# Kernel tuning notes

Hardware: AMD Instinct MI355X
Metric: run time of the kernel (lower is better)

Reference implementation:

```python
import jax, jax.numpy as jnp
import numpy as np

N_ENT = 50000
N_EDGE = 500000
H_DIM = 128
N_REL_TAB = 475  # 2*n_rel + 1


def setup_inputs() -> dict:
    key = jax.random.key(0)
    ks = jax.random.split(key, 8)
    scale = 1.0 / np.sqrt(H_DIM)
    return {
        "ent_emb": jax.random.normal(ks[0], (N_ENT, H_DIM), jnp.float32) * scale,
        "rel_emb": jax.random.normal(ks[1], (N_REL_TAB, H_DIM), jnp.float32) * scale,
        "w_edge": jax.random.normal(ks[2], (H_DIM, H_DIM), jnp.float32) * scale,
        "w_node": jax.random.normal(ks[3], (H_DIM, H_DIM), jnp.float32) * scale,
        "w_comp": jax.random.normal(ks[4], (H_DIM, H_DIM), jnp.float32) * scale,
        "src": jax.random.randint(ks[5], (N_EDGE,), 0, N_ENT, jnp.int32),
        "dst": jax.random.randint(ks[6], (N_EDGE,), 0, N_ENT, jnp.int32),
        "rel_id": jax.random.randint(ks[7], (N_EDGE,), 0, N_REL_TAB - 1, jnp.int32),
    }


def _edge_softmax(logits, dst, n_nodes):
    # dgl.ops.edge_softmax: softmax over incoming edges of each destination node
    m = jax.ops.segment_max(logits, dst, num_segments=n_nodes)  # (N,)
    ex = jnp.exp(logits - m[dst])                               # (E,)
    s = jax.ops.segment_sum(ex, dst, num_segments=n_nodes)     # (N,)
    return ex / s[dst]


def _attn_aggregate(msg, key_emb_dst, dst, n_nodes, w):
    # norm = e_dot_v, edge_softmax, weighted scatter-sum, GEMM, Tanh
    logits = jnp.sum(msg * key_emb_dst, axis=-1)                # (E,)
    a = _edge_softmax(logits, dst, n_nodes)                     # (E,)
    neigh = jax.ops.segment_sum(msg * a[:, None], dst, num_segments=n_nodes)  # (N,H)
    return jnp.tanh(neigh @ w)


def reference(ent_emb, rel_emb, w_edge, w_node, w_comp, src, dst, rel_id):
    n = ent_emb.shape[0]
    v = ent_emb[dst]            # (E,H) destination node emb (shared key for all layers)
    u = ent_emb[src]            # (E,H)
    r = rel_emb[rel_id]         # (E,H)

    # EdgeLayer: message = rel emb
    edge_out = _attn_aggregate(r, v, dst, n, w_edge)
    # NodeLayer: message = src node emb (u_dot_v logits, u_mul_e aggregation)
    node_out = _attn_aggregate(u, v, dst, n, w_node)
    # CompLayer (comp_op='add'): message = u + rel emb
    comp_out = _attn_aggregate(u + r, v, dst, n, w_comp)

    return ent_emb + edge_out + node_out + comp_out
```

## Files before the change

kernel.cpp:

```cpp
#include <hip/hip_runtime.h>
#include <math.h>

#define N_ENT   50000
#define N_REL   475
#define N_EDGE  500000
#define HD      128
#define CAP     64

typedef unsigned int u32;
typedef __attribute__((ext_vector_type(8))) short short8;
typedef __attribute__((ext_vector_type(4))) float f32x4;
typedef __attribute__((ext_vector_type(2))) float f32x2;
typedef __attribute__((ext_vector_type(4))) u32 u32x4;

__device__ __forceinline__ u32 bf16_1(float f) {
  u32 u = __float_as_uint(f);
  return (u + 0x7fffu + ((u >> 16) & 1u)) >> 16;
}
__device__ __forceinline__ u32 bf16_pack(float lo, float hi) {
  return bf16_1(lo) | (bf16_1(hi) << 16);
}
__device__ __forceinline__ float bf_lo(u32 w) { return __uint_as_float(w << 16); }
__device__ __forceinline__ float bf_hi(u32 w) { return __uint_as_float(w & 0xffff0000u); }
__device__ __forceinline__ f32x2 bf2(u32 w) { return (f32x2){bf_lo(w), bf_hi(w)}; }
__device__ __forceinline__ float fast_tanh(float x) {
  float e = __expf(2.f * x);
  return 1.f - 2.f * __builtin_amdgcn_rcpf(e + 1.f);
}

#define DEG_BLKS ((N_EDGE + 255) / 256)
#define CVT_ITEMS ((N_ENT + N_REL) * 16 + 3 * 8 * 4 * 64)
#define CVT_BLKS ((CVT_ITEMS + 255) / 256)

__global__ void k_degree_cvt(const int* __restrict__ dst, const int* __restrict__ src,
                             const int* __restrict__ rel, int* __restrict__ counts,
                             u32* __restrict__ psru,
                             const float* __restrict__ ent, const float* __restrict__ relw,
                             const float* __restrict__ we, const float* __restrict__ wn,
                             const float* __restrict__ wc, u32* __restrict__ ent16,
                             u32* __restrict__ rel16, u32* __restrict__ wpack) {
  int b = blockIdx.x;
  if (b < DEG_BLKS) {
    int e = b * 256 + threadIdx.x;
    if (e < N_EDGE) {
      int d = dst[e];
      int slot = atomicAdd(&counts[d], 1);
      if (slot > CAP - 1) slot = CAP - 1;
      psru[(size_t)d * CAP + slot] = (u32)src[e] | ((u32)rel[e] << 16);
    }
    return;
  }
  int t = (b - DEG_BLKS) * 256 + threadIdx.x;
  const int CVT = (N_ENT + N_REL) * 16;
  if (t < CVT) {
    int row = t >> 4, seg = t & 15;
    const float* s;
    u32* d;
    if (row < N_ENT) {
      s = ent + (size_t)row * HD + seg * 8;
      d = ent16 + (size_t)row * 64 + seg * 4;
    } else {
      int rr = row - N_ENT;
      s = relw + (size_t)rr * HD + seg * 8;
      d = rel16 + (size_t)rr * 64 + seg * 4;
    }
    float4 A = *(const float4*)s, B = *(const float4*)(s + 4);
    u32x4 o = {bf16_pack(A.x, A.y), bf16_pack(A.z, A.w),
               bf16_pack(B.x, B.y), bf16_pack(B.z, B.w)};
    *(u32x4*)d = o;
  } else if (t < CVT_ITEMS) {
    int idx = t - CVT;
    int lane = idx & 63, ks = (idx >> 6) & 3, ct = (idx >> 8) & 7, l = idx >> 11;
    const float* W = (l == 0) ? we : (l == 1) ? wn : wc;
    int c = ct * 16 + (lane & 15);
    int kb = ks * 32 + (lane >> 4) * 8;
    u32x4 o;
#pragma unroll
    for (int jp = 0; jp < 4; ++jp) {
      int k0 = kb + 2 * jp;
      o[jp] = bf16_pack(W[k0 * HD + c], W[(k0 + 1) * HD + c]);
    }
    *(u32x4*)(wpack + idx * 4) = o;
  }
}

__global__ __launch_bounds__(256) void k_aggregate(
    const u32* __restrict__ ent16, const u32* __restrict__ rel16,
    const int* __restrict__ counts, const u32* __restrict__ psru,
    u32* __restrict__ neighb) {
  int lane = threadIdx.x & 63;
  int node = blockIdx.x * 4 + (threadIdx.x >> 6);
  int grp = lane >> 4, gl = lane & 15;

  u32x4 V = *(const u32x4*)(ent16 + (size_t)node * 64 + gl * 4);
  f32x2 vv2[4];
#pragma unroll
  for (int k = 0; k < 4; ++k) vv2[k] = bf2(V[k]);

  f32x2 Su = {0.f, 0.f};
  float S2 = 0.f;
  f32x2 a0[4], a1[4], a2[4];
#pragma unroll
  for (int k = 0; k < 4; ++k) a0[k] = a1[k] = a2[k] = (f32x2){0.f, 0.f};

  int cnt = counts[node];
  if (cnt > CAP) cnt = CAP;
  int e0 = node * CAP, e1 = e0 + cnt;
  if (e0 < e1) {
    int elast = e1 - 1;
    auto fetch = [&](int eb, u32x4& U, u32x4& R) {
      int e = eb + grp;
      u32 p = psru[(e < e1) ? e : elast];
      U = *(const u32x4*)(ent16 + (size_t)(p & 0xFFFFu) * 64 + gl * 4);
      R = *(const u32x4*)(rel16 + (size_t)(p >> 16) * 64 + gl * 4);
    };
    auto process = [&](u32x4& U, u32x4& R, int eb) {
      f32x2 cu2[4], cr2[4];
#pragma unroll
      for (int k = 0; k < 4; ++k) { cu2[k] = bf2(U[k]); cr2[k] = bf2(R[k]); }
      fetch(eb + 12, U, R);
      bool valid = (eb + grp < e1);
      f32x2 du2 = {0.f, 0.f}, dq2 = {0.f, 0.f};
#pragma unroll
      for (int k = 0; k < 4; ++k) {
        du2 += cu2[k] * vv2[k];
        dq2 += cr2[k] * vv2[k];
      }
      f32x2 p = {du2.x + du2.y, dq2.x + dq2.y};
#pragma unroll
      for (int off = 1; off < 16; off <<= 1) {
        f32x2 t;
        t.x = __shfl_xor(p.x, off, 64);
        t.y = __shfl_xor(p.y, off, 64);
        p += t;
      }
      float e_u = valid ? __expf(p.x) : 0.f;
      float e_r = valid ? __expf(p.y) : 0.f;
      float e_c = e_u * e_r;
      Su += (f32x2){e_r, e_u};
      S2 += e_c;
      f32x2 er2 = {e_r, e_r}, eu2 = {e_u, e_u}, ec2 = {e_c, e_c};
#pragma unroll
      for (int k = 0; k < 4; ++k) {
        a0[k] += er2 * cr2[k];
        a1[k] += eu2 * cu2[k];
        a2[k] += ec2 * (cu2[k] + cr2[k]);
      }
    };
    u32x4 uA, rA, uB, rB, uC, rC;
    fetch(e0, uA, rA);
    fetch(e0 + 4, uB, rB);
    fetch(e0 + 8, uC, rC);
    int eb = e0;
    for (; eb + 8 < e1; eb += 12) {
      process(uA, rA, eb);
      process(uB, rB, eb + 4);
      process(uC, rC, eb + 8);
    }
    if (eb < e1) process(uA, rA, eb);
    if (eb + 4 < e1) process(uB, rB, eb + 4);
  }

  {
    f32x2 t;
    t.x = __shfl_xor(Su.x, 16, 64); t.y = __shfl_xor(Su.y, 16, 64); Su += t;
    t.x = __shfl_xor(Su.x, 32, 64); t.y = __shfl_xor(Su.y, 32, 64); Su += t;
    S2 += __shfl_xor(S2, 16, 64); S2 += __shfl_xor(S2, 32, 64);
  }
  float w0 = (Su.x > 0.f) ? __builtin_amdgcn_rcpf(Su.x) : 0.f;
  float w1 = (Su.y > 0.f) ? __builtin_amdgcn_rcpf(Su.y) : 0.f;
  float w2 = (S2 > 0.f) ? __builtin_amdgcn_rcpf(S2) : 0.f;
#pragma unroll
  for (int k = 0; k < 4; ++k) {
    f32x2 t;
    t.x = __shfl_xor(a0[k].x, 16, 64); t.y = __shfl_xor(a0[k].y, 16, 64); a0[k] += t;
    t.x = __shfl_xor(a0[k].x, 32, 64); t.y = __shfl_xor(a0[k].y, 32, 64); a0[k] += t;
    t.x = __shfl_xor(a1[k].x, 16, 64); t.y = __shfl_xor(a1[k].y, 16, 64); a1[k] += t;
    t.x = __shfl_xor(a1[k].x, 32, 64); t.y = __shfl_xor(a1[k].y, 32, 64); a1[k] += t;
    t.x = __shfl_xor(a2[k].x, 16, 64); t.y = __shfl_xor(a2[k].y, 16, 64); a2[k] += t;
    t.x = __shfl_xor(a2[k].x, 32, 64); t.y = __shfl_xor(a2[k].y, 32, 64); a2[k] += t;
  }

  int base = node * 64 + gl * 4;
  if (grp == 0) {
    u32x4 o = {bf16_pack(a0[0].x * w0, a0[0].y * w0), bf16_pack(a0[1].x * w0, a0[1].y * w0),
               bf16_pack(a0[2].x * w0, a0[2].y * w0), bf16_pack(a0[3].x * w0, a0[3].y * w0)};
    *(u32x4*)(neighb + base) = o;
  } else if (grp == 1) {
    u32x4 o = {bf16_pack(a1[0].x * w1, a1[0].y * w1), bf16_pack(a1[1].x * w1, a1[1].y * w1),
               bf16_pack(a1[2].x * w1, a1[2].y * w1), bf16_pack(a1[3].x * w1, a1[3].y * w1)};
    *(u32x4*)(neighb + N_ENT * 64 + base) = o;
  } else if (grp == 2) {
    u32x4 o = {bf16_pack(a2[0].x * w2, a2[0].y * w2), bf16_pack(a2[1].x * w2, a2[1].y * w2),
               bf16_pack(a2[2].x * w2, a2[2].y * w2), bf16_pack(a2[3].x * w2, a2[3].y * w2)};
    *(u32x4*)(neighb + 2 * N_ENT * 64 + base) = o;
  }
}

__global__ __launch_bounds__(256) void k_out(
    const float* __restrict__ ent, const u32* __restrict__ neighb,
    const u32* __restrict__ wpack, float* __restrict__ out) {
  int lane = threadIdx.x & 63, wv = threadIdx.x >> 6;
  int n0 = blockIdx.x * 64 + wv * 16;

  int arow = n0 + (lane & 15);
  int arow_c = (arow < N_ENT) ? arow : 0;
  int ko2 = (lane >> 4) * 4;

  f32x4 res[8];
#pragma unroll
  for (int t = 0; t < 8; ++t) res[t] = (f32x4){0.f, 0.f, 0.f, 0.f};

#pragma unroll
  for (int l = 0; l < 3; ++l) {
    const u32* nb = neighb + (size_t)l * (N_ENT * 64);
    short8 a[4];
#pragma unroll
    for (int ks = 0; ks < 4; ++ks)
      a[ks] = *(const short8*)(nb + (size_t)arow_c * 64 + ks * 16 + ko2);
    const u32* wp = wpack + l * 8192;
#pragma unroll
    for (int ct = 0; ct < 8; ++ct) {
      f32x4 acc = (f32x4){0.f, 0.f, 0.f, 0.f};
#pragma unroll
      for (int ks = 0; ks < 4; ++ks) {
        short8 b = *(const short8*)(wp + ((ct * 4 + ks) * 64 + lane) * 4);
        acc = __builtin_amdgcn_mfma_f32_16x16x32_bf16(a[ks], b, acc, 0, 0, 0);
      }
#pragma unroll
      for (int r = 0; r < 4; ++r) res[ct][r] += fast_tanh(acc[r]);
    }
  }
  int rbase = n0 + (lane >> 4) * 4;
  int cbase = lane & 15;
#pragma unroll
  for (int ct = 0; ct < 8; ++ct) {
    int col = ct * 16 + cbase;
#pragma unroll
    for (int r = 0; r < 4; ++r) {
      int row = rbase + r;
      if (row < N_ENT)
        out[(size_t)row * HD + col] = ent[(size_t)row * HD + col] + res[ct][r];
    }
  }
}

extern "C" void kernel_launch(void* const* d_in, const int* in_sizes, int n_in,
                              void* d_out, int out_size, void* d_ws, size_t ws_size,
                              hipStream_t stream) {
  const float* ent = (const float*)d_in[0];
  const float* rel = (const float*)d_in[1];
  const float* w_e = (const float*)d_in[2];
  const float* w_n = (const float*)d_in[3];
  const float* w_c = (const float*)d_in[4];
  const int* src = (const int*)d_in[5];
  const int* dst = (const int*)d_in[6];
  const int* relid = (const int*)d_in[7];
  float* out = (float*)d_out;

  char* ws = (char*)d_ws;
  size_t off = 0;
  auto alloc = [&](size_t bytes) {
    void* p = ws + off;
    off = (off + bytes + 255) & ~(size_t)255;
    return p;
  };
  int* counts = (int*)alloc((size_t)N_ENT * 4);
  u32* psru = (u32*)alloc((size_t)N_ENT * CAP * 4);
  u32* ent16 = (u32*)alloc((size_t)N_ENT * 64 * 4);
  u32* rel16 = (u32*)alloc((size_t)N_REL * 64 * 4);
  u32* neighb = (u32*)alloc(3ull * N_ENT * 64 * 4);
  u32* wpack = (u32*)alloc((size_t)3 * 8 * 4 * 64 * 4 * 4);
  (void)ws_size; (void)in_sizes; (void)n_in; (void)out_size;

  hipMemsetAsync(counts, 0, (size_t)N_ENT * 4, stream);

  k_degree_cvt<<<DEG_BLKS + CVT_BLKS, 256, 0, stream>>>(dst, src, relid, counts, psru,
                                                        ent, rel, w_e, w_n, w_c, ent16,
                                                        rel16, wpack);
  k_aggregate<<<N_ENT / 4, 256, 0, stream>>>(ent16, rel16, counts, psru, neighb);
  k_out<<<(N_ENT + 63) / 64, 256, 0, stream>>>(ent, neighb, wpack, out);
}
```

Measured before the change: 215.4 us.

## Fuse neighbor aggregation and output GEMM into one kernel via LDS slab

Merges the aggregation kernel and the MFMA output kernel into a single kernel. Each wave now aggregates 16 nodes one after another and stages their bf16 neighbor sums in a padded LDS slab, then runs the three GEMMs with tanh straight from LDS. This removes the global write and re-read of the intermediate neighbor buffer and one kernel launch. In exchange, far fewer waves are in flight to hide gather latency, and the odd LDS stride breaks 16-byte alignment of the vector LDS accesses.

```diff
diff --git a/kernel.cpp b/kernel.cpp
--- a/kernel.cpp
+++ b/kernel.cpp
@@ -31,6 +31,7 @@
 #define DEG_BLKS ((N_EDGE + 255) / 256)
 #define CVT_ITEMS ((N_ENT + N_REL) * 16 + 3 * 8 * 4 * 64)
 #define CVT_BLKS ((CVT_ITEMS + 255) / 256)
+#define NSTRIDE 193
 
 __global__ void k_degree_cvt(const int* __restrict__ dst, const int* __restrict__ src,
                              const int* __restrict__ rel, int* __restrict__ counts,
@@ -84,128 +85,126 @@
   }
 }
 
-__global__ __launch_bounds__(256) void k_aggregate(
+__global__ __launch_bounds__(256) void k_agg_out(
     const u32* __restrict__ ent16, const u32* __restrict__ rel16,
     const int* __restrict__ counts, const u32* __restrict__ psru,
-    u32* __restrict__ neighb) {
-  int lane = threadIdx.x & 63;
-  int node = blockIdx.x * 4 + (threadIdx.x >> 6);
+    const float* __restrict__ ent, const u32* __restrict__ wpack,
+    float* __restrict__ out) {
+  __shared__ u32 slab[4][16 * NSTRIDE];
+  int lane = threadIdx.x & 63, wv = threadIdx.x >> 6;
   int grp = lane >> 4, gl = lane & 15;
-
-  u32x4 V = *(const u32x4*)(ent16 + (size_t)node * 64 + gl * 4);
-  f32x2 vv2[4];
-#pragma unroll
-  for (int k = 0; k < 4; ++k) vv2[k] = bf2(V[k]);
-
-  f32x2 Su = {0.f, 0.f};
-  float S2 = 0.f;
-  f32x2 a0[4], a1[4], a2[4];
-#pragma unroll
-  for (int k = 0; k < 4; ++k) a0[k] = a1[k] = a2[k] = (f32x2){0.f, 0.f};
-
-  int cnt = counts[node];
-  if (cnt > CAP) cnt = CAP;
-  int e0 = node * CAP, e1 = e0 + cnt;
-  if (e0 < e1) {
-    int elast = e1 - 1;
-    auto fetch = [&](int eb, u32x4& U, u32x4& R) {
-      int e = eb + grp;
-      u32 p = psru[(e < e1) ? e : elast];
-      U = *(const u32x4*)(ent16 + (size_t)(p & 0xFFFFu) * 64 + gl * 4);
-      R = *(const u32x4*)(rel16 + (size_t)(p >> 16) * 64 + gl * 4);
-    };
-    auto process = [&](u32x4& U, u32x4& R, int eb) {
-      f32x2 cu2[4], cr2[4];
-#pragma unroll
-      for (int k = 0; k < 4; ++k) { cu2[k] = bf2(U[k]); cr2[k] = bf2(R[k]); }
-      fetch(eb + 12, U, R);
-      bool valid = (eb + grp < e1);
-      f32x2 du2 = {0.f, 0.f}, dq2 = {0.f, 0.f};
-#pragma unroll
-      for (int k = 0; k < 4; ++k) {
-        du2 += cu2[k] * vv2[k];
-        dq2 += cr2[k] * vv2[k];
+  int nbase = blockIdx.x * 64 + wv * 16;
+  u32* wslab = &slab[wv][0];
+
+  for (int i = 0; i < 16; ++i) {
+    int node = nbase + i;
+    bool nvalid = (node < N_ENT);
+    int nclamp = nvalid ? node : N_ENT - 1;
+
+    u32x4 V = *(const u32x4*)(ent16 + (size_t)nclamp * 64 + gl * 4);
+    f32x2 vv2[4];
+#pragma unroll
+    for (int k = 0; k < 4; ++k) vv2[k] = bf2(V[k]);
+
+    f32x2 Su = {0.f, 0.f};
+    float S2 = 0.f;
+    f32x2 a0[4], a1[4], a2[4];
+#pragma unroll
+    for (int k = 0; k < 4; ++k) a0[k] = a1[k] = a2[k] = (f32x2){0.f, 0.f};
+
+    int cnt = nvalid ? counts[node] : 0;
+    if (cnt > CAP) cnt = CAP;
+    int e0 = nclamp * CAP, e1 = e0 + cnt;
+    if (e0 < e1) {
+      int elast = e1 - 1;
+      auto fetch = [&](int eb, u32x4& U, u32x4& R) {
+        int e = eb + grp;
+        u32 p = psru[(e < e1) ? e : elast];
+        U = *(const u32x4*)(ent16 + (size_t)(p & 0xFFFFu) * 64 + gl * 4);
+        R = *(const u32x4*)(rel16 + (size_t)(p >> 16) * 64 + gl * 4);
+      };
+      auto process = [&](u32x4& U, u32x4& R, int eb) {
+        f32x2 cu2[4], cr2[4];
+#pragma unroll
+        for (int k = 0; k < 4; ++k) { cu2[k] = bf2(U[k]); cr2[k] = bf2(R[k]); }
+        fetch(eb + 12, U, R);
+        bool valid = (eb + grp < e1);
+        f32x2 du2 = {0.f, 0.f}, dq2 = {0.f, 0.f};
+#pragma unroll
+        for (int k = 0; k < 4; ++k) {
+          du2 += cu2[k] * vv2[k];
+          dq2 += cr2[k] * vv2[k];
+        }
+        f32x2 p = {du2.x + du2.y, dq2.x + dq2.y};
+#pragma unroll
+        for (int off = 1; off < 16; off <<= 1) {
+          f32x2 t;
+          t.x = __shfl_xor(p.x, off, 64);
+          t.y = __shfl_xor(p.y, off, 64);
+          p += t;
+        }
+        float e_u = valid ? __expf(p.x) : 0.f;
+        float e_r = valid ? __expf(p.y) : 0.f;
+        float e_c = e_u * e_r;
+        Su += (f32x2){e_r, e_u};
+        S2 += e_c;
+        f32x2 er2 = {e_r, e_r}, eu2 = {e_u, e_u}, ec2 = {e_c, e_c};
+#pragma unroll
+        for (int k = 0; k < 4; ++k) {
+          a0[k] += er2 * cr2[k];
+          a1[k] += eu2 * cu2[k];
+          a2[k] += ec2 * (cu2[k] + cr2[k]);
+        }
+      };
+      u32x4 uA, rA, uB, rB, uC, rC;
+      fetch(e0, uA, rA);
+      fetch(e0 + 4, uB, rB);
+      fetch(e0 + 8, uC, rC);
+      int eb = e0;
+      for (; eb + 8 < e1; eb += 12) {
+        process(uA, rA, eb);
+        process(uB, rB, eb + 4);
+        process(uC, rC, eb + 8);
       }
-      f32x2 p = {du2.x + du2.y, dq2.x + dq2.y};
-#pragma unroll
-      for (int off = 1; off < 16; off <<= 1) {
-        f32x2 t;
-        t.x = __shfl_xor(p.x, off, 64);
-        t.y = __shfl_xor(p.y, off, 64);
-        p += t;
-      }
-      float e_u = valid ? __expf(p.x) : 0.f;
-      float e_r = valid ? __expf(p.y) : 0.f;
-      float e_c = e_u * e_r;
-      Su += (f32x2){e_r, e_u};
-      S2 += e_c;
-      f32x2 er2 = {e_r, e_r}, eu2 = {e_u, e_u}, ec2 = {e_c, e_c};
-#pragma unroll
-      for (int k = 0; k < 4; ++k) {
-        a0[k] += er2 * cr2[k];
-        a1[k] += eu2 * cu2[k];
-        a2[k] += ec2 * (cu2[k] + cr2[k]);
-      }
-    };
-    u32x4 uA, rA, uB, rB, uC, rC;
-    fetch(e0, uA, rA);
-    fetch(e0 + 4, uB, rB);
-    fetch(e0 + 8, uC, rC);
-    int eb = e0;
-    for (; eb + 8 < e1; eb += 12) {
-      process(uA, rA, eb);
-      process(uB, rB, eb + 4);
-      process(uC, rC, eb + 8);
-    }
-    if (eb < e1) process(uA, rA, eb);
-    if (eb + 4 < e1) process(uB, rB, eb + 4);
-  }
-
-  {
-    f32x2 t;
-    t.x = __shfl_xor(Su.x, 16, 64); t.y = __shfl_xor(Su.y, 16, 64); Su += t;
-    t.x = __shfl_xor(Su.x, 32, 64); t.y = __shfl_xor(Su.y, 32, 64); Su += t;
-    S2 += __shfl_xor(S2, 16, 64); S2 += __shfl_xor(S2, 32, 64);
-  }
-  float w0 = (Su.x > 0.f) ? __builtin_amdgcn_rcpf(Su.x) : 0.f;
-  float w1 = (Su.y > 0.f) ? __builtin_amdgcn_rcpf(Su.y) : 0.f;
-  float w2 = (S2 > 0.f) ? __builtin_amdgcn_rcpf(S2) : 0.f;
-#pragma unroll
-  for (int k = 0; k < 4; ++k) {
-    f32x2 t;
-    t.x = __shfl_xor(a0[k].x, 16, 64); t.y = __shfl_xor(a0[k].y, 16, 64); a0[k] += t;
-    t.x = __shfl_xor(a0[k].x, 32, 64); t.y = __shfl_xor(a0[k].y, 32, 64); a0[k] += t;
-    t.x = __shfl_xor(a1[k].x, 16, 64); t.y = __shfl_xor(a1[k].y, 16, 64); a1[k] += t;
-    t.x = __shfl_xor(a1[k].x, 32, 64); t.y = __shfl_xor(a1[k].y, 32, 64); a1[k] += t;
-    t.x = __shfl_xor(a2[k].x, 16, 64); t.y = __shfl_xor(a2[k].y, 16, 64); a2[k] += t;
-    t.x = __shfl_xor(a2[k].x, 32, 64); t.y = __shfl_xor(a2[k].y, 32, 64); a2[k] += t;
-  }
-
-  int base = node * 64 + gl * 4;
-  if (grp == 0) {
-    u32x4 o = {bf16_pack(a0[0].x * w0, a0[0].y * w0), bf16_pack(a0[1].x * w0, a0[1].y * w0),
-               bf16_pack(a0[2].x * w0, a0[2].y * w0), bf16_pack(a0[3].x * w0, a0[3].y * w0)};
-    *(u32x4*)(neighb + base) = o;
-  } else if (grp == 1) {
-    u32x4 o = {bf16_pack(a1[0].x * w1, a1[0].y * w1), bf16_pack(a1[1].x * w1, a1[1].y * w1),
-               bf16_pack(a1[2].x * w1, a1[2].y * w1), bf16_pack(a1[3].x * w1, a1[3].y * w1)};
-    *(u32x4*)(neighb + N_ENT * 64 + base) = o;
-  } else if (grp == 2) {
-    u32x4 o = {bf16_pack(a2[0].x * w2, a2[0].y * w2), bf16_pack(a2[1].x * w2, a2[1].y * w2),
-               bf16_pack(a2[2].x * w2, a2[2].y * w2), bf16_pack(a2[3].x * w2, a2[3].y * w2)};
-    *(u32x4*)(neighb + 2 * N_ENT * 64 + base) = o;
-  }
-}
-
-__global__ __launch_bounds__(256) void k_out(
-    const float* __restrict__ ent, const u32* __restrict__ neighb,
-    const u32* __restrict__ wpack, float* __restrict__ out) {
-  int lane = threadIdx.x & 63, wv = threadIdx.x >> 6;
-  int n0 = blockIdx.x * 64 + wv * 16;
-
-  int arow = n0 + (lane & 15);
-  int arow_c = (arow < N_ENT) ? arow : 0;
-  int ko2 = (lane >> 4) * 4;
+      if (eb < e1) process(uA, rA, eb);
+      if (eb + 4 < e1) process(uB, rB, eb + 4);
+    }
+
+    {
+      f32x2 t;
+      t.x = __shfl_xor(Su.x, 16, 64); t.y = __shfl_xor(Su.y, 16, 64); Su += t;
+      t.x = __shfl_xor(Su.x, 32, 64); t.y = __shfl_xor(Su.y, 32, 64); Su += t;
+      S2 += __shfl_xor(S2, 16, 64); S2 += __shfl_xor(S2, 32, 64);
+    }
+    float w0 = (Su.x > 0.f) ? __builtin_amdgcn_rcpf(Su.x) : 0.f;
+    float w1 = (Su.y > 0.f) ? __builtin_amdgcn_rcpf(Su.y) : 0.f;
+    float w2 = (S2 > 0.f) ? __builtin_amdgcn_rcpf(S2) : 0.f;
+#pragma unroll
+    for (int k = 0; k < 4; ++k) {
+      f32x2 t;
+      t.x = __shfl_xor(a0[k].x, 16, 64); t.y = __shfl_xor(a0[k].y, 16, 64); a0[k] += t;
+      t.x = __shfl_xor(a0[k].x, 32, 64); t.y = __shfl_xor(a0[k].y, 32, 64); a0[k] += t;
+      t.x = __shfl_xor(a1[k].x, 16, 64); t.y = __shfl_xor(a1[k].y, 16, 64); a1[k] += t;
+      t.x = __shfl_xor(a1[k].x, 32, 64); t.y = __shfl_xor(a1[k].y, 32, 64); a1[k] += t;
+      t.x = __shfl_xor(a2[k].x, 16, 64); t.y = __shfl_xor(a2[k].y, 16, 64); a2[k] += t;
+      t.x = __shfl_xor(a2[k].x, 32, 64); t.y = __shfl_xor(a2[k].y, 32, 64); a2[k] += t;
+    }
+
+    u32* srow = wslab + i * NSTRIDE + grp * 64 + gl * 4;
+    if (grp == 0) {
+      u32x4 o = {bf16_pack(a0[0].x * w0, a0[0].y * w0), bf16_pack(a0[1].x * w0, a0[1].y * w0),
+                 bf16_pack(a0[2].x * w0, a0[2].y * w0), bf16_pack(a0[3].x * w0, a0[3].y * w0)};
+      *(u32x4*)srow = o;
+    } else if (grp == 1) {
+      u32x4 o = {bf16_pack(a1[0].x * w1, a1[0].y * w1), bf16_pack(a1[1].x * w1, a1[1].y * w1),
+                 bf16_pack(a1[2].x * w1, a1[2].y * w1), bf16_pack(a1[3].x * w1, a1[3].y * w1)};
+      *(u32x4*)srow = o;
+    } else if (grp == 2) {
+      u32x4 o = {bf16_pack(a2[0].x * w2, a2[0].y * w2), bf16_pack(a2[1].x * w2, a2[1].y * w2),
+                 bf16_pack(a2[2].x * w2, a2[2].y * w2), bf16_pack(a2[3].x * w2, a2[3].y * w2)};
+      *(u32x4*)srow = o;
+    }
+  }
 
   f32x4 res[8];
 #pragma unroll
@@ -213,11 +212,11 @@
 
 #pragma unroll
   for (int l = 0; l < 3; ++l) {
-    const u32* nb = neighb + (size_t)l * (N_ENT * 64);
     short8 a[4];
 #pragma unroll
     for (int ks = 0; ks < 4; ++ks)
-      a[ks] = *(const short8*)(nb + (size_t)arow_c * 64 + ks * 16 + ko2);
+      a[ks] = *(const short8*)(wslab + (lane & 15) * NSTRIDE + l * 64 + ks * 16 +
+                               (lane >> 4) * 4);
     const u32* wp = wpack + l * 8192;
 #pragma unroll
     for (int ct = 0; ct < 8; ++ct) {
@@ -231,7 +230,7 @@
       for (int r = 0; r < 4; ++r) res[ct][r] += fast_tanh(acc[r]);
     }
   }
-  int rbase = n0 + (lane >> 4) * 4;
+  int rbase = nbase + (lane >> 4) * 4;
   int cbase = lane & 15;
 #pragma unroll
   for (int ct = 0; ct < 8; ++ct) {
@@ -269,7 +268,6 @@
   u32* psru = (u32*)alloc((size_t)N_ENT * CAP * 4);
   u32* ent16 = (u32*)alloc((size_t)N_ENT * 64 * 4);
   u32* rel16 = (u32*)alloc((size_t)N_REL * 64 * 4);
-  u32* neighb = (u32*)alloc(3ull * N_ENT * 64 * 4);
   u32* wpack = (u32*)alloc((size_t)3 * 8 * 4 * 64 * 4 * 4);
   (void)ws_size; (void)in_sizes; (void)n_in; (void)out_size;
 
@@ -278,6 +276,6 @@
   k_degree_cvt<<<DEG_BLKS + CVT_BLKS, 256, 0, stream>>>(dst, src, relid, counts, psru,
                                                         ent, rel, w_e, w_n, w_c, ent16,
                                                         rel16, wpack);
-  k_aggregate<<<N_ENT / 4, 256, 0, stream>>>(ent16, rel16, counts, psru, neighb);
-  k_out<<<(N_ENT + 63) / 64, 256, 0, stream>>>(ent, neighb, wpack, out);
-}
+  k_agg_out<<<(N_ENT + 63) / 64, 256, 0, stream>>>(ent16, rel16, counts, psru, ent,
+                                                   wpack, out);
+}
```

After: 265.6 us. 23.3% more time.
